# Kernel tuning notes

Measured on AMD Instinct MI355X. Metric: run time of the kernel, lower is better.

## Reference

```python
import jax, jax.numpy as jnp
import numpy as np

B, T, H = 512, 256, 1024


def setup_inputs() -> dict:
    key = jax.random.key(0)
    ks = jax.random.split(key, 7)
    s = 1.0 / np.sqrt(H)
    return {
        "x": jax.random.normal(ks[0], (B, T), dtype=jnp.float32),
        "W_ih": jax.random.normal(ks[1], (4 * H, 1), dtype=jnp.float32) * s,
        "W_hh": jax.random.normal(ks[2], (4 * H, H), dtype=jnp.float32) * s,
        "b_ih": jax.random.normal(ks[3], (4 * H,), dtype=jnp.float32) * s,
        "b_hh": jax.random.normal(ks[4], (4 * H,), dtype=jnp.float32) * s,
        "W_out": jax.random.normal(ks[5], (1, H), dtype=jnp.float32) * s,
        "b_out": jax.random.normal(ks[6], (1,), dtype=jnp.float32) * s,
    }


def reference(x, W_ih, W_hh, b_ih, b_hh, W_out, b_out):
    # x: [B, T]; LSTMCell recurrence over T with a linear head per step.
    Bx, Tx = x.shape
    Hh = W_hh.shape[1]
    b = b_ih + b_hh  # [4H]
    xs = x.T[:, :, None]  # [T, B, 1] timestep slices

    def step(carry, x_t):
        h, c = carry
        # gates: [B, 4H] = x_t @ W_ih^T + h @ W_hh^T + b (torch LSTMCell order i,f,g,o)
        gates = x_t @ W_ih.T + h @ W_hh.T + b
        i, f, g, o = jnp.split(gates, 4, axis=-1)
        i = jax.nn.sigmoid(i)
        f = jax.nn.sigmoid(f)
        g = jnp.tanh(g)
        o = jax.nn.sigmoid(o)
        c = f * c + i * g
        h = o * jnp.tanh(c)
        out = h @ W_out.T + b_out  # [B, 1]
        return (h, c), out

    h0 = jnp.zeros((Bx, Hh), dtype=x.dtype)
    c0 = jnp.zeros((Bx, Hh), dtype=x.dtype)
    _, outs = jax.lax.scan(step, (h0, c0), xs)  # outs: [T, B, 1]
    # torch.stack(outputs, 1).squeeze(2) -> [B, T]
    return outs[:, :, 0].T
```

## Files before the change

### kernel.cpp

```cpp
#include <hip/hip_runtime.h>
#include <hip/hip_fp16.h>
#include <hip/hip_cooperative_groups.h>

#define B_ 512
#define T_ 256
#define H_ 1024
#define G4_ 4096
#define KL_ 20
#define KG_ 12

typedef _Float16 half8 __attribute__((ext_vector_type(8)));
typedef float f32x4 __attribute__((ext_vector_type(4)));

__device__ __forceinline__ float fast_sigmoid(float x) {
    return 1.0f / (1.0f + __expf(-x));
}
__device__ __forceinline__ float fast_tanh(float x) {
    float x2 = fminf(fmaxf(2.0f * x, -30.0f), 30.0f);
    float e = __expf(x2);
    return (e - 1.0f) / (e + 1.0f);
}

__global__ void pack_w(const float* __restrict__ Whh,
                       _Float16* __restrict__ Wlds, _Float16* __restrict__ Wl2) {
    int idx = blockIdx.x * blockDim.x + threadIdx.x;
    int gc = idx >> 10, k = idx & 1023;
    int nt = gc >> 10, u = gc & 1023;
    int jb = u >> 4, lk = u & 15;
    int ki = k >> 5, hi = (k >> 3) & 3, e = k & 7;
    int l = hi * 16 + lk;
    _Float16 v = (_Float16)Whh[idx];
    int frag = nt * 512 + l * 8 + e;
    if (ki < KL_) {
        int slot = jb >> 1, wj = jb & 1;
        Wlds[(size_t)slot * 81920 + wj * 40960 + ki * 2048 + frag] = v;
    } else {
        Wl2[(size_t)jb * 24576 + (ki - KL_) * 2048 + frag] = v;
    }
}

__global__ void init_misc(const float* __restrict__ bih, const float* __restrict__ bhh,
                          const float* __restrict__ bout,
                          float* __restrict__ bias, float* __restrict__ out) {
    int idx = blockIdx.x * blockDim.x + threadIdx.x;
    if (idx < G4_) bias[idx] = bih[idx] + bhh[idx];
    if (idx < B_ * T_) out[idx] = bout[0];
}

__global__ __launch_bounds__(512, 1)
void lstm_persist(const _Float16* __restrict__ Wlds,
                  const _Float16* __restrict__ Wl2,
                  const float* __restrict__ bias,
                  const float* __restrict__ x,
                  const float* __restrict__ Wih,
                  const float* __restrict__ Wout,
                  _Float16* __restrict__ hbuf,
                  float* __restrict__ out,
                  unsigned int* __restrict__ cnts) {
    extern __shared__ _Float16 Wl[];
    cooperative_groups::grid_group grid = cooperative_groups::this_grid();

    const int tid = threadIdx.x;
    unsigned int xcc;
    asm volatile("s_getreg_b32 %0, hwreg(HW_REG_XCC_ID)" : "=s"(xcc));
    const int xcd = (int)(xcc & 7u);
    if (tid == 0) {
        unsigned int s = __hip_atomic_fetch_add(&cnts[xcd], 1u,
                                                __ATOMIC_RELAXED, __HIP_MEMORY_SCOPE_AGENT);
        __hip_atomic_store(&cnts[512 + blockIdx.x], s,
                           __ATOMIC_RELAXED, __HIP_MEMORY_SCOPE_AGENT);
    }
    grid.sync();
    const int slot = (int)__hip_atomic_load(&cnts[512 + blockIdx.x],
                                            __ATOMIC_RELAXED, __HIP_MEMORY_SCOPE_AGENT);
    const int nactive = (int)min(32u, __hip_atomic_load(&cnts[xcd], __ATOMIC_RELAXED,
                                                        __HIP_MEMORY_SCOPE_AGENT));
    if (slot >= 32) return;

    const int w = tid >> 6, l = tid & 63;
    const int lk = l & 15, hi = l >> 4;
    const int wr = w >> 1, wj = w & 1;
    const int row0 = wr * 16;
    const int u = slot * 32 + wj * 16 + lk;

    {
        const half8* src = (const half8*)(Wlds + (size_t)slot * 81920);
        half8* dst = (half8*)Wl;
#pragma unroll
        for (int o = 0; o < 20; ++o) dst[tid + o * 512] = src[tid + o * 512];
    }
    float bz[4], wi4[4];
#pragma unroll
    for (int nt = 0; nt < 4; ++nt) {
        int gc = nt * 1024 + u;
        bz[nt] = bias[gc];
        wi4[nt] = Wih[gc];
    }
    const float wout = Wout[u];
    int rowsl[4], rowsg[4];
#pragma unroll
    for (int r = 0; r < 4; ++r) {
        rowsl[r] = row0 + hi * 4 + r;
        rowsg[r] = xcd * 64 + rowsl[r];
    }
    const int kb = u >> 3, ue = u & 7;
    f32x4 creg = {0.f, 0.f, 0.f, 0.f};
    __syncthreads();

    _Float16* hx = hbuf + (size_t)xcd * 2 * 65536;
    const _Float16* Bg = Wl2 + ((size_t)slot * 2 + wj) * 24576 + l * 8;
    unsigned int* barp = &cnts[16 + xcd * 32];

    for (int t = 0; t < T_; ++t) {
        const int wb = t & 1, rb = wb ^ 1;
        f32x4 acc[4];
        float xv[4];
#pragma unroll
        for (int r = 0; r < 4; ++r) xv[r] = x[rowsg[r] * T_ + t];
#pragma unroll
        for (int nt = 0; nt < 4; ++nt) {
#pragma unroll
            for (int r = 0; r < 4; ++r) acc[nt][r] = bz[nt] + xv[r] * wi4[nt];
        }

        if (t > 0) {
            const _Float16* Ap = hx + rb * 65536 + hi * 512 + (row0 + lk) * 8;
#pragma unroll
            for (int kg = 0; kg < KG_; ++kg) {
                half8 a = *(const half8*)(Ap + (KL_ + kg) * 2048);
                const _Float16* bp = Bg + kg * 2048;
#pragma unroll
                for (int nt = 0; nt < 4; ++nt) {
                    half8 b = *(const half8*)(bp + nt * 512);
                    acc[nt] = __builtin_amdgcn_mfma_f32_16x16x32_f16(a, b, acc[nt], 0, 0, 0);
                }
            }
#pragma unroll
            for (int ki = 0; ki < KL_; ++ki) {
                half8 a = *(const half8*)(Ap + ki * 2048);
                const _Float16* bp = Wl + wj * 40960 + ki * 2048 + l * 8;
#pragma unroll
                for (int nt = 0; nt < 4; ++nt) {
                    half8 b = *(const half8*)(bp + nt * 512);
                    acc[nt] = __builtin_amdgcn_mfma_f32_16x16x32_f16(a, b, acc[nt], 0, 0, 0);
                }
            }
        }

        _Float16* hn = hx + wb * 65536;
        float p4[4];
#pragma unroll
        for (int r = 0; r < 4; ++r) {
            float iv = fast_sigmoid(acc[0][r]);
            float fv = fast_sigmoid(acc[1][r]);
            float gv = fast_tanh(acc[2][r]);
            float ov = fast_sigmoid(acc[3][r]);
            float cv = fv * creg[r] + iv * gv;
            creg[r] = cv;
            float hv = ov * fast_tanh(cv);
            hn[(kb * 64 + rowsl[r]) * 8 + ue] = (_Float16)hv;
            p4[r] = hv * wout;
        }
#pragma unroll
        for (int m = 1; m <= 8; m <<= 1) {
#pragma unroll
            for (int r = 0; r < 4; ++r) p4[r] += __shfl_xor(p4[r], m);
        }
        if (lk == 0) {
#pragma unroll
            for (int r = 0; r < 4; ++r)
                atomicAdd(&out[rowsg[r] * T_ + t], p4[r]);
        }

        if (t < T_ - 1) {
            __syncthreads();
            if (tid == 0) {
                __hip_atomic_fetch_add(barp, 1u, __ATOMIC_RELAXED, __HIP_MEMORY_SCOPE_AGENT);
                unsigned int tgt = (unsigned int)nactive * (unsigned int)(t + 1);
                while (__hip_atomic_load(barp, __ATOMIC_RELAXED, __HIP_MEMORY_SCOPE_AGENT) < tgt)
                    __builtin_amdgcn_s_sleep(2);
            }
            __syncthreads();
            asm volatile("buffer_inv sc0" ::: "memory");
        }
    }
}

extern "C" void kernel_launch(void* const* d_in, const int* in_sizes, int n_in,
                              void* d_out, int out_size, void* d_ws, size_t ws_size,
                              hipStream_t stream) {
    const float* x    = (const float*)d_in[0];
    const float* Wih  = (const float*)d_in[1];
    const float* Whh  = (const float*)d_in[2];
    const float* bih  = (const float*)d_in[3];
    const float* bhh  = (const float*)d_in[4];
    const float* Wout = (const float*)d_in[5];
    const float* bout = (const float*)d_in[6];
    float* out = (float*)d_out;

    char* ws = (char*)d_ws;
    _Float16* Wlds = (_Float16*)ws;
    _Float16* Wl2  = (_Float16*)(ws + 5242880);
    _Float16* hbuf = (_Float16*)(ws + (8 << 20));
    float* bias    = (float*)(ws + (10 << 20));
    unsigned int* cnts = (unsigned int*)(ws + (10 << 20) + (64 << 10));

    hipMemsetAsync(cnts, 0, 4096, stream);
    pack_w<<<(G4_ * H_) / 256, 256, 0, stream>>>(Whh, Wlds, Wl2);
    init_misc<<<512, 256, 0, stream>>>(bih, bhh, bout, bias, out);

    (void)hipFuncSetAttribute((const void*)lstm_persist,
                              hipFuncAttributeMaxDynamicSharedMemorySize, 163840);
    void* args[] = {&Wlds, &Wl2, &bias, &x, &Wih, &Wout, &hbuf, &out, &cnts};
    hipLaunchCooperativeKernel((void*)lstm_persist, dim3(256), dim3(512),
                               args, 163840, stream);
}
```

Measured before the change: 2.082 ms.

## Keep part of the global-resident weight slice in registers and prefetch the rest

Eight of the twelve K-groups of recurrent weights that did not fit in LDS are now loaded once into registers before the time loop, so they are no longer re-read from global/L2 every step. The remaining four K-groups are prefetched into registers in two batches ahead of the LDS-fed MFMA loops, which hides their latency behind LDS work. The reordering changes the accumulation order. The large register array (32 half8 plus prefetch buffers) raises VGPR pressure, and launch_bounds is changed to (512,2), which may cap registers and cause spills.

Result: faster. 1.881 ms (-9.7%).

```diff
diff --git a/kernel.cpp b/kernel.cpp
--- a/kernel.cpp
+++ b/kernel.cpp
@@ -7,7 +7,8 @@
 #define H_ 1024
 #define G4_ 4096
 #define KL_ 20
-#define KG_ 12
+#define KR_ 8
+#define KS_ 4
 
 typedef _Float16 half8 __attribute__((ext_vector_type(8)));
 typedef float f32x4 __attribute__((ext_vector_type(4)));
@@ -47,7 +48,7 @@
     if (idx < B_ * T_) out[idx] = bout[0];
 }
 
-__global__ __launch_bounds__(512, 1)
+__global__ __launch_bounds__(512, 2)
 void lstm_persist(const _Float16* __restrict__ Wlds,
                   const _Float16* __restrict__ Wl2,
                   const float* __restrict__ bias,
@@ -89,6 +90,14 @@
 #pragma unroll
         for (int o = 0; o < 20; ++o) dst[tid + o * 512] = src[tid + o * 512];
     }
+    const _Float16* Bg = Wl2 + ((size_t)slot * 2 + wj) * 24576 + l * 8;
+    half8 breg[KR_ * 4];
+#pragma unroll
+    for (int kg = 0; kg < KR_; ++kg)
+#pragma unroll
+        for (int nt = 0; nt < 4; ++nt)
+            breg[kg * 4 + nt] = *(const half8*)(Bg + kg * 2048 + nt * 512);
+
     float bz[4], wi4[4];
 #pragma unroll
     for (int nt = 0; nt < 4; ++nt) {
@@ -108,7 +117,7 @@
     __syncthreads();
 
     _Float16* hx = hbuf + (size_t)xcd * 2 * 65536;
-    const _Float16* Bg = Wl2 + ((size_t)slot * 2 + wj) * 24576 + l * 8;
+    const _Float16* Bgs = Bg + KR_ * 2048;
     unsigned int* barp = &cnts[16 + xcd * 32];
 
     for (int t = 0; t < T_; ++t) {
@@ -125,18 +134,26 @@
 
         if (t > 0) {
             const _Float16* Ap = hx + rb * 65536 + hi * 512 + (row0 + lk) * 8;
-#pragma unroll
-            for (int kg = 0; kg < KG_; ++kg) {
-                half8 a = *(const half8*)(Ap + (KL_ + kg) * 2048);
-                const _Float16* bp = Bg + kg * 2048;
+            half8 bs[8];
+#pragma unroll
+            for (int q = 0; q < 8; ++q)
+                bs[q] = *(const half8*)(Bgs + (q >> 2) * 2048 + (q & 3) * 512);
+#pragma unroll
+            for (int ki = 0; ki < 10; ++ki) {
+                half8 a = *(const half8*)(Ap + ki * 2048);
+                const _Float16* bp = Wl + wj * 40960 + ki * 2048 + l * 8;
 #pragma unroll
                 for (int nt = 0; nt < 4; ++nt) {
                     half8 b = *(const half8*)(bp + nt * 512);
                     acc[nt] = __builtin_amdgcn_mfma_f32_16x16x32_f16(a, b, acc[nt], 0, 0, 0);
                 }
             }
-#pragma unroll
-            for (int ki = 0; ki < KL_; ++ki) {
+            half8 bs2[8];
+#pragma unroll
+            for (int q = 0; q < 8; ++q)
+                bs2[q] = *(const half8*)(Bgs + (2 + (q >> 2)) * 2048 + (q & 3) * 512);
+#pragma unroll
+            for (int ki = 10; ki < KL_; ++ki) {
                 half8 a = *(const half8*)(Ap + ki * 2048);
                 const _Float16* bp = Wl + wj * 40960 + ki * 2048 + l * 8;
 #pragma unroll
@@ -144,6 +161,27 @@
                     half8 b = *(const half8*)(bp + nt * 512);
                     acc[nt] = __builtin_amdgcn_mfma_f32_16x16x32_f16(a, b, acc[nt], 0, 0, 0);
                 }
+            }
+#pragma unroll
+            for (int kg = 0; kg < KR_; ++kg) {
+                half8 a = *(const half8*)(Ap + (KL_ + kg) * 2048);
+#pragma unroll
+                for (int nt = 0; nt < 4; ++nt)
+                    acc[nt] = __builtin_amdgcn_mfma_f32_16x16x32_f16(a, breg[kg * 4 + nt], acc[nt], 0, 0, 0);
+            }
+#pragma unroll
+            for (int kg = 0; kg < 2; ++kg) {
+                half8 a = *(const half8*)(Ap + (KL_ + KR_ + kg) * 2048);
+#pragma unroll
+                for (int nt = 0; nt < 4; ++nt)
+                    acc[nt] = __builtin_amdgcn_mfma_f32_16x16x32_f16(a, bs[kg * 4 + nt], acc[nt], 0, 0, 0);
+            }
+#pragma unroll
+            for (int kg = 0; kg < 2; ++kg) {
+                half8 a = *(const half8*)(Ap + (KL_ + KR_ + 2 + kg) * 2048);
+#pragma unroll
+                for (int nt = 0; nt < 4; ++nt)
+                    acc[nt] = __builtin_amdgcn_mfma_f32_16x16x32_f16(a, bs2[kg * 4 + nt], acc[nt], 0, 0, 0);
             }
         }
 
```

## Halve block size with two row tiles per wave and split-phase barrier

Applied to the files above, without the earlier changes.

Each block now runs 256 threads, and every wave handles two 16-row M tiles. This lets each weight fragment loaded from LDS or global memory feed two MFMAs, doubling reuse. The global weight fragments are prefetched into registers in chunks, interleaved with the LDS-resident k-blocks. The inter-block barrier is split: a block signals arrival right after writing h, does the output reduction, atomics and next-step x load, and only then waits at the start of the next step. The cooperative launch and grid.sync are replaced by a plain launch with a hand-rolled atomic start barrier, which assumes all 256 blocks are co-resident. The change also raises register pressure.

Result: slower. 3.075 ms (+47.7%).

```diff
diff --git a/kernel.cpp b/kernel.cpp
--- a/kernel.cpp
+++ b/kernel.cpp
@@ -1,6 +1,5 @@
 #include <hip/hip_runtime.h>
 #include <hip/hip_fp16.h>
-#include <hip/hip_cooperative_groups.h>
 
 #define B_ 512
 #define T_ 256
@@ -47,7 +46,7 @@
     if (idx < B_ * T_) out[idx] = bout[0];
 }
 
-__global__ __launch_bounds__(512, 1)
+__global__ __launch_bounds__(256, 1)
 void lstm_persist(const _Float16* __restrict__ Wlds,
                   const _Float16* __restrict__ Wl2,
                   const float* __restrict__ bias,
@@ -58,7 +57,6 @@
                   float* __restrict__ out,
                   unsigned int* __restrict__ cnts) {
     extern __shared__ _Float16 Wl[];
-    cooperative_groups::grid_group grid = cooperative_groups::this_grid();
 
     const int tid = threadIdx.x;
     unsigned int xcc;
@@ -69,8 +67,11 @@
                                                 __ATOMIC_RELAXED, __HIP_MEMORY_SCOPE_AGENT);
         __hip_atomic_store(&cnts[512 + blockIdx.x], s,
                            __ATOMIC_RELAXED, __HIP_MEMORY_SCOPE_AGENT);
-    }
-    grid.sync();
+        __hip_atomic_fetch_add(&cnts[8], 1u, __ATOMIC_ACQ_REL, __HIP_MEMORY_SCOPE_AGENT);
+        while (__hip_atomic_load(&cnts[8], __ATOMIC_ACQUIRE, __HIP_MEMORY_SCOPE_AGENT) < 256u)
+            __builtin_amdgcn_s_sleep(2);
+    }
+    __syncthreads();
     const int slot = (int)__hip_atomic_load(&cnts[512 + blockIdx.x],
                                             __ATOMIC_RELAXED, __HIP_MEMORY_SCOPE_AGENT);
     const int nactive = (int)min(32u, __hip_atomic_load(&cnts[xcd], __ATOMIC_RELAXED,
@@ -80,14 +81,14 @@
     const int w = tid >> 6, l = tid & 63;
     const int lk = l & 15, hi = l >> 4;
     const int wr = w >> 1, wj = w & 1;
-    const int row0 = wr * 16;
+    const int row0 = wr * 32;
     const int u = slot * 32 + wj * 16 + lk;
 
     {
         const half8* src = (const half8*)(Wlds + (size_t)slot * 81920);
         half8* dst = (half8*)Wl;
 #pragma unroll
-        for (int o = 0; o < 20; ++o) dst[tid + o * 512] = src[tid + o * 512];
+        for (int o = 0; o < 40; ++o) dst[tid + o * 256] = src[tid + o * 256];
     }
     float bz[4], wi4[4];
 #pragma unroll
@@ -97,91 +98,134 @@
         wi4[nt] = Wih[gc];
     }
     const float wout = Wout[u];
-    int rowsl[4], rowsg[4];
+    int rowsl[8], rowsg[8];
+#pragma unroll
+    for (int s = 0; s < 2; ++s)
 #pragma unroll
     for (int r = 0; r < 4; ++r) {
-        rowsl[r] = row0 + hi * 4 + r;
-        rowsg[r] = xcd * 64 + rowsl[r];
+        rowsl[s * 4 + r] = row0 + s * 16 + hi * 4 + r;
+        rowsg[s * 4 + r] = xcd * 64 + rowsl[s * 4 + r];
     }
     const int kb = u >> 3, ue = u & 7;
-    f32x4 creg = {0.f, 0.f, 0.f, 0.f};
+    f32x4 creg[2] = {{0.f, 0.f, 0.f, 0.f}, {0.f, 0.f, 0.f, 0.f}};
     __syncthreads();
 
     _Float16* hx = hbuf + (size_t)xcd * 2 * 65536;
     const _Float16* Bg = Wl2 + ((size_t)slot * 2 + wj) * 24576 + l * 8;
     unsigned int* barp = &cnts[16 + xcd * 32];
 
+    float xv[8];
+#pragma unroll
+    for (int i = 0; i < 8; ++i) xv[i] = x[rowsg[i] * T_];
+
     for (int t = 0; t < T_; ++t) {
-        const int wb = t & 1, rb = wb ^ 1;
-        f32x4 acc[4];
-        float xv[4];
-#pragma unroll
-        for (int r = 0; r < 4; ++r) xv[r] = x[rowsg[r] * T_ + t];
-#pragma unroll
-        for (int nt = 0; nt < 4; ++nt) {
-#pragma unroll
-            for (int r = 0; r < 4; ++r) acc[nt][r] = bz[nt] + xv[r] * wi4[nt];
-        }
-
         if (t > 0) {
-            const _Float16* Ap = hx + rb * 65536 + hi * 512 + (row0 + lk) * 8;
-#pragma unroll
-            for (int kg = 0; kg < KG_; ++kg) {
-                half8 a = *(const half8*)(Ap + (KL_ + kg) * 2048);
-                const _Float16* bp = Bg + kg * 2048;
-#pragma unroll
-                for (int nt = 0; nt < 4; ++nt) {
-                    half8 b = *(const half8*)(bp + nt * 512);
-                    acc[nt] = __builtin_amdgcn_mfma_f32_16x16x32_f16(a, b, acc[nt], 0, 0, 0);
-                }
-            }
-#pragma unroll
-            for (int ki = 0; ki < KL_; ++ki) {
-                half8 a = *(const half8*)(Ap + ki * 2048);
-                const _Float16* bp = Wl + wj * 40960 + ki * 2048 + l * 8;
-#pragma unroll
-                for (int nt = 0; nt < 4; ++nt) {
-                    half8 b = *(const half8*)(bp + nt * 512);
-                    acc[nt] = __builtin_amdgcn_mfma_f32_16x16x32_f16(a, b, acc[nt], 0, 0, 0);
-                }
-            }
-        }
-
-        _Float16* hn = hx + wb * 65536;
-        float p4[4];
-#pragma unroll
-        for (int r = 0; r < 4; ++r) {
-            float iv = fast_sigmoid(acc[0][r]);
-            float fv = fast_sigmoid(acc[1][r]);
-            float gv = fast_tanh(acc[2][r]);
-            float ov = fast_sigmoid(acc[3][r]);
-            float cv = fv * creg[r] + iv * gv;
-            creg[r] = cv;
-            float hv = ov * fast_tanh(cv);
-            hn[(kb * 64 + rowsl[r]) * 8 + ue] = (_Float16)hv;
-            p4[r] = hv * wout;
-        }
-#pragma unroll
-        for (int m = 1; m <= 8; m <<= 1) {
-#pragma unroll
-            for (int r = 0; r < 4; ++r) p4[r] += __shfl_xor(p4[r], m);
-        }
-        if (lk == 0) {
-#pragma unroll
-            for (int r = 0; r < 4; ++r)
-                atomicAdd(&out[rowsg[r] * T_ + t], p4[r]);
-        }
-
-        if (t < T_ - 1) {
-            __syncthreads();
             if (tid == 0) {
-                __hip_atomic_fetch_add(barp, 1u, __ATOMIC_RELAXED, __HIP_MEMORY_SCOPE_AGENT);
-                unsigned int tgt = (unsigned int)nactive * (unsigned int)(t + 1);
+                unsigned int tgt = (unsigned int)nactive * (unsigned int)t;
                 while (__hip_atomic_load(barp, __ATOMIC_RELAXED, __HIP_MEMORY_SCOPE_AGENT) < tgt)
                     __builtin_amdgcn_s_sleep(2);
             }
             __syncthreads();
             asm volatile("buffer_inv sc0" ::: "memory");
+        }
+
+        const int wb = t & 1, rb = wb ^ 1;
+        f32x4 acc[2][4];
+#pragma unroll
+        for (int s = 0; s < 2; ++s)
+#pragma unroll
+        for (int nt = 0; nt < 4; ++nt)
+#pragma unroll
+        for (int r = 0; r < 4; ++r)
+            acc[s][nt][r] = bz[nt] + xv[s * 4 + r] * wi4[nt];
+
+        if (t > 0) {
+            const _Float16* Ap0 = hx + rb * 65536 + hi * 512 + (row0 + lk) * 8;
+            const _Float16* Ap1 = Ap0 + 128;
+            half8 bb[16];
+
+#define LOADB(KG0) \
+    _Pragma("unroll") \
+    for (int q = 0; q < 16; ++q) \
+        bb[q] = *(const half8*)(Bg + (KG0 + (q >> 2)) * 2048 + (q & 3) * 512);
+
+#define LDSBLK(K0, K1) \
+    _Pragma("unroll") \
+    for (int ki = K0; ki < K1; ++ki) { \
+        half8 a0 = *(const half8*)(Ap0 + ki * 2048); \
+        half8 a1 = *(const half8*)(Ap1 + ki * 2048); \
+        const _Float16* bp = Wl + wj * 40960 + ki * 2048 + l * 8; \
+        _Pragma("unroll") \
+        for (int nt = 0; nt < 4; ++nt) { \
+            half8 b = *(const half8*)(bp + nt * 512); \
+            acc[0][nt] = __builtin_amdgcn_mfma_f32_16x16x32_f16(a0, b, acc[0][nt], 0, 0, 0); \
+            acc[1][nt] = __builtin_amdgcn_mfma_f32_16x16x32_f16(a1, b, acc[1][nt], 0, 0, 0); \
+        } \
+    }
+
+#define CONSB(KG0) \
+    _Pragma("unroll") \
+    for (int kg = 0; kg < 4; ++kg) { \
+        half8 a0 = *(const half8*)(Ap0 + (KL_ + KG0 + kg) * 2048); \
+        half8 a1 = *(const half8*)(Ap1 + (KL_ + KG0 + kg) * 2048); \
+        _Pragma("unroll") \
+        for (int nt = 0; nt < 4; ++nt) { \
+            acc[0][nt] = __builtin_amdgcn_mfma_f32_16x16x32_f16(a0, bb[kg * 4 + nt], acc[0][nt], 0, 0, 0); \
+            acc[1][nt] = __builtin_amdgcn_mfma_f32_16x16x32_f16(a1, bb[kg * 4 + nt], acc[1][nt], 0, 0, 0); \
+        } \
+    }
+
+            LOADB(0)
+            LDSBLK(0, 10)
+            CONSB(0)
+            LOADB(4)
+            LDSBLK(10, 16)
+            CONSB(4)
+            LOADB(8)
+            LDSBLK(16, 20)
+            CONSB(8)
+#undef LOADB
+#undef LDSBLK
+#undef CONSB
+        }
+
+        _Float16* hn = hx + wb * 65536;
+        float p8[8];
+#pragma unroll
+        for (int s = 0; s < 2; ++s)
+#pragma unroll
+        for (int r = 0; r < 4; ++r) {
+            int i = s * 4 + r;
+            float iv = fast_sigmoid(acc[s][0][r]);
+            float fv = fast_sigmoid(acc[s][1][r]);
+            float gv = fast_tanh(acc[s][2][r]);
+            float ov = fast_sigmoid(acc[s][3][r]);
+            float cv = fv * creg[s][r] + iv * gv;
+            creg[s][r] = cv;
+            float hv = ov * fast_tanh(cv);
+            hn[(kb * 64 + rowsl[i]) * 8 + ue] = (_Float16)hv;
+            p8[i] = hv * wout;
+        }
+
+        if (t < T_ - 1) {
+            __syncthreads();
+            if (tid == 0)
+                __hip_atomic_fetch_add(barp, 1u, __ATOMIC_RELAXED, __HIP_MEMORY_SCOPE_AGENT);
+        }
+
+#pragma unroll
+        for (int m = 1; m <= 8; m <<= 1) {
+#pragma unroll
+            for (int i = 0; i < 8; ++i) p8[i] += __shfl_xor(p8[i], m);
+        }
+        if (lk == 0) {
+#pragma unroll
+            for (int i = 0; i < 8; ++i)
+                atomicAdd(&out[rowsg[i] * T_ + t], p8[i]);
+        }
+        if (t < T_ - 1) {
+#pragma unroll
+            for (int i = 0; i < 8; ++i) xv[i] = x[rowsg[i] * T_ + t + 1];
         }
     }
 }
@@ -211,7 +255,6 @@
 
     (void)hipFuncSetAttribute((const void*)lstm_persist,
                               hipFuncAttributeMaxDynamicSharedMemorySize, 163840);
-    void* args[] = {&Wlds, &Wl2, &bias, &x, &Wih, &Wout, &hbuf, &out, &cnts};
-    hipLaunchCooperativeKernel((void*)lstm_persist, dim3(256), dim3(512),
-                               args, 163840, stream);
-}
+    lstm_persist<<<dim3(256), dim3(256), 163840, stream>>>(
+        Wlds, Wl2, bias, x, Wih, Wout, hbuf, out, cnts);
+}
```

## Split barrier into arrive/wait and prefetch next-step weights and inputs

Applied to the files above, without the earlier changes.

Splits the per-step inter-block barrier into an arrive right after h is written and a wait at the top of the next step, so the output reduction, atomics, and prefetch of the next x values and the first global weight fragments overlap the barrier latency. Global-memory weight loads are batched into 20-register groups to raise memory-level parallelism. The cooperative launch and grid.sync are replaced by a plain launch with a hand-rolled atomic startup barrier. The costs are higher register pressure and reliance on all 256 blocks being co-resident without the cooperative-launch guarantee.

New measurement: 2.161 ms. +3.8%, slower.

```diff
diff --git a/kernel.cpp b/kernel.cpp
--- a/kernel.cpp
+++ b/kernel.cpp
@@ -1,6 +1,5 @@
 #include <hip/hip_runtime.h>
 #include <hip/hip_fp16.h>
-#include <hip/hip_cooperative_groups.h>
 
 #define B_ 512
 #define T_ 256
@@ -8,6 +7,7 @@
 #define G4_ 4096
 #define KL_ 20
 #define KG_ 12
+#define PRE_ 2
 
 typedef _Float16 half8 __attribute__((ext_vector_type(8)));
 typedef float f32x4 __attribute__((ext_vector_type(4)));
@@ -58,7 +58,6 @@
                   float* __restrict__ out,
                   unsigned int* __restrict__ cnts) {
     extern __shared__ _Float16 Wl[];
-    cooperative_groups::grid_group grid = cooperative_groups::this_grid();
 
     const int tid = threadIdx.x;
     unsigned int xcc;
@@ -69,8 +68,11 @@
                                                 __ATOMIC_RELAXED, __HIP_MEMORY_SCOPE_AGENT);
         __hip_atomic_store(&cnts[512 + blockIdx.x], s,
                            __ATOMIC_RELAXED, __HIP_MEMORY_SCOPE_AGENT);
-    }
-    grid.sync();
+        __hip_atomic_fetch_add(&cnts[8], 1u, __ATOMIC_ACQ_REL, __HIP_MEMORY_SCOPE_AGENT);
+        while (__hip_atomic_load(&cnts[8], __ATOMIC_ACQUIRE, __HIP_MEMORY_SCOPE_AGENT) < 256u)
+            __builtin_amdgcn_s_sleep(2);
+    }
+    __syncthreads();
     const int slot = (int)__hip_atomic_load(&cnts[512 + blockIdx.x],
                                             __ATOMIC_RELAXED, __HIP_MEMORY_SCOPE_AGENT);
     const int nactive = (int)min(32u, __hip_atomic_load(&cnts[xcd], __ATOMIC_RELAXED,
@@ -111,12 +113,25 @@
     const _Float16* Bg = Wl2 + ((size_t)slot * 2 + wj) * 24576 + l * 8;
     unsigned int* barp = &cnts[16 + xcd * 32];
 
+    float xv[4];
+#pragma unroll
+    for (int r = 0; r < 4; ++r) xv[r] = x[rowsg[r] * T_];
+
+    half8 bbp[PRE_ * 4];
+
     for (int t = 0; t < T_; ++t) {
+        if (t > 0) {
+            if (tid == 0) {
+                unsigned int tgt = (unsigned int)nactive * (unsigned int)t;
+                while (__hip_atomic_load(barp, __ATOMIC_RELAXED, __HIP_MEMORY_SCOPE_AGENT) < tgt)
+                    __builtin_amdgcn_s_sleep(2);
+            }
+            __syncthreads();
+            asm volatile("buffer_inv sc0" ::: "memory");
+        }
+
         const int wb = t & 1, rb = wb ^ 1;
         f32x4 acc[4];
-        float xv[4];
-#pragma unroll
-        for (int r = 0; r < 4; ++r) xv[r] = x[rowsg[r] * T_ + t];
 #pragma unroll
         for (int nt = 0; nt < 4; ++nt) {
 #pragma unroll
@@ -125,17 +140,36 @@
 
         if (t > 0) {
             const _Float16* Ap = hx + rb * 65536 + hi * 512 + (row0 + lk) * 8;
-#pragma unroll
-            for (int kg = 0; kg < KG_; ++kg) {
+
+#pragma unroll
+            for (int kg = 0; kg < PRE_; ++kg) {
                 half8 a = *(const half8*)(Ap + (KL_ + kg) * 2048);
-                const _Float16* bp = Bg + kg * 2048;
-#pragma unroll
-                for (int nt = 0; nt < 4; ++nt) {
-                    half8 b = *(const half8*)(bp + nt * 512);
-                    acc[nt] = __builtin_amdgcn_mfma_f32_16x16x32_f16(a, b, acc[nt], 0, 0, 0);
-                }
-            }
-#pragma unroll
+#pragma unroll
+                for (int nt = 0; nt < 4; ++nt)
+                    acc[nt] = __builtin_amdgcn_mfma_f32_16x16x32_f16(a, bbp[kg * 4 + nt], acc[nt], 0, 0, 0);
+            }
+            half8 bb[20];
+#pragma unroll
+            for (int q = 0; q < 20; ++q)
+                bb[q] = *(const half8*)(Bg + (PRE_ + (q >> 2)) * 2048 + (q & 3) * 512);
+#pragma unroll
+            for (int kg = 0; kg < 5; ++kg) {
+                half8 a = *(const half8*)(Ap + (KL_ + PRE_ + kg) * 2048);
+#pragma unroll
+                for (int nt = 0; nt < 4; ++nt)
+                    acc[nt] = __builtin_amdgcn_mfma_f32_16x16x32_f16(a, bb[kg * 4 + nt], acc[nt], 0, 0, 0);
+            }
+#pragma unroll
+            for (int q = 0; q < 20; ++q)
+                bb[q] = *(const half8*)(Bg + (PRE_ + 5 + (q >> 2)) * 2048 + (q & 3) * 512);
+#pragma unroll
+            for (int kg = 0; kg < 5; ++kg) {
+                half8 a = *(const half8*)(Ap + (KL_ + PRE_ + 5 + kg) * 2048);
+#pragma unroll
+                for (int nt = 0; nt < 4; ++nt)
+                    acc[nt] = __builtin_amdgcn_mfma_f32_16x16x32_f16(a, bb[kg * 4 + nt], acc[nt], 0, 0, 0);
+            }
+#pragma unroll 5
             for (int ki = 0; ki < KL_; ++ki) {
                 half8 a = *(const half8*)(Ap + ki * 2048);
                 const _Float16* bp = Wl + wj * 40960 + ki * 2048 + l * 8;
@@ -161,6 +195,13 @@
             hn[(kb * 64 + rowsl[r]) * 8 + ue] = (_Float16)hv;
             p4[r] = hv * wout;
         }
+
+        if (t < T_ - 1) {
+            __syncthreads();
+            if (tid == 0)
+                __hip_atomic_fetch_add(barp, 1u, __ATOMIC_RELAXED, __HIP_MEMORY_SCOPE_AGENT);
+        }
+
 #pragma unroll
         for (int m = 1; m <= 8; m <<= 1) {
 #pragma unroll
@@ -171,17 +212,12 @@
             for (int r = 0; r < 4; ++r)
                 atomicAdd(&out[rowsg[r] * T_ + t], p4[r]);
         }
-
         if (t < T_ - 1) {
-            __syncthreads();
-            if (tid == 0) {
-                __hip_atomic_fetch_add(barp, 1u, __ATOMIC_RELAXED, __HIP_MEMORY_SCOPE_AGENT);
-                unsigned int tgt = (unsigned int)nactive * (unsigned int)(t + 1);
-                while (__hip_atomic_load(barp, __ATOMIC_RELAXED, __HIP_MEMORY_SCOPE_AGENT) < tgt)
-                    __builtin_amdgcn_s_sleep(2);
-            }
-            __syncthreads();
-            asm volatile("buffer_inv sc0" ::: "memory");
+#pragma unroll
+            for (int r = 0; r < 4; ++r) xv[r] = x[rowsg[r] * T_ + t + 1];
+#pragma unroll
+            for (int q = 0; q < PRE_ * 4; ++q)
+                bbp[q] = *(const half8*)(Bg + (q >> 2) * 2048 + (q & 3) * 512);
         }
     }
 }
@@ -211,7 +247,6 @@
 
     (void)hipFuncSetAttribute((const void*)lstm_persist,
                               hipFuncAttributeMaxDynamicSharedMemorySize, 163840);
-    void* args[] = {&Wlds, &Wl2, &bias, &x, &Wih, &Wout, &hbuf, &out, &cnts};
-    hipLaunchCooperativeKernel((void*)lstm_persist, dim3(256), dim3(512),
-                               args, 163840, stream);
-}
+    lstm_persist<<<dim3(256), dim3(512), 163840, stream>>>(
+        Wlds, Wl2, bias, x, Wih, Wout, hbuf, out, cnts);
+}
```
